# Kernel tuning notes

Hardware: AMD Instinct MI355X
Metric: run time of the kernel (lower is better)

Reference implementation:

```python
import jax, jax.numpy as jnp
import numpy as np
from jax import lax

B, T, N, D = 8, 64, 197, 768
HID = 4
K_FRAME, K_TOKEN = 8, 49
LAMBDA_COV, LAMBDA_SCORE = 1.0, 0.5
LN_EPS = 1e-5


def setup_inputs() -> dict:
    key = jax.random.key(0)
    k = jax.random.split(key, 5)
    x = jax.random.normal(k[0], (B, T, N, D), jnp.float32)
    mask = jax.random.uniform(k[1], (B, T, N), jnp.float32)
    ln_gamma = jnp.ones((D,), jnp.float32)
    ln_beta = jnp.zeros((D,), jnp.float32)
    W1 = jax.random.normal(k[2], (D, HID * D), jnp.float32) * 0.02
    b1 = jnp.zeros((HID * D,), jnp.float32)
    W2 = jax.random.normal(k[3], (HID * D, 1), jnp.float32) * 0.02
    b2 = jnp.zeros((1,), jnp.float32)
    return {"x": x, "mask": mask, "ln_gamma": ln_gamma, "ln_beta": ln_beta,
            "W1": W1, "b1": b1, "W2": W2, "b2": b2}


def _facility_location(frame_repr, score, valid, k):
    # cosine similarity between frames (F.normalize eps = 1e-12)
    fn = frame_repr / jnp.clip(jnp.linalg.norm(frame_repr, axis=-1, keepdims=True), 1e-12)
    sim = jnp.einsum('bid,bjd->bij', fn, fn)  # [B,T,T]
    Bb, Tt = score.shape

    def step(carry, _):
        best_cover, chosen = carry  # [B,T], [B,T] bool
        # coverage gain per candidate j: sum_i max(best[i], sim[i,j]) - best[i]
        cov_gain = jnp.maximum(best_cover[:, :, None], sim).sum(1) - best_cover.sum(1, keepdims=True)
        total = LAMBDA_COV * cov_gain + LAMBDA_SCORE * score
        total = jnp.where(valid & (~chosen), total, -jnp.inf)
        j = jnp.argmax(total, axis=1)  # [B]
        sim_j = jnp.take_along_axis(sim, j[:, None, None], axis=2)[..., 0]  # [B,T]
        best_cover = jnp.maximum(best_cover, sim_j)
        chosen = chosen.at[jnp.arange(Bb), j].set(True)
        return (best_cover, chosen), j

    init = (jnp.zeros((Bb, Tt), frame_repr.dtype), jnp.zeros((Bb, Tt), bool))
    (_, chosen), js = lax.scan(step, init, None, length=k)
    return js.T, chosen.astype(frame_repr.dtype)  # frame_idx [B,k], frame_mask [B,T]


def _kcenter(X, valid, k):
    # X [N,D], valid [N] bool; greedy k-center (farthest point sampling)
    d0 = jnp.where(valid, (X * X).sum(-1), -jnp.inf)
    first = jnp.argmax(d0)

    def dist_to(i):
        diff = X - X[i]
        return jnp.sqrt((diff * diff).sum(-1))

    min_dist = jnp.where(valid, dist_to(first), -1.0)

    def step(md, _):
        cand = jnp.argmax(md)
        md = jnp.where(valid, jnp.minimum(md, dist_to(cand)), -1.0)
        return md, cand

    _, rest = lax.scan(step, min_dist, None, length=k - 1)
    return jnp.concatenate([first[None], rest])


def _forward(x, mask, ln_gamma, ln_beta, W1, b1, W2, b2):
    # masked mean frame representation (use_cls=False path)
    denom = jnp.clip(mask.sum(2), 1e-6)                      # [B,T]
    frame_repr = (x * mask[..., None]).sum(2) / denom[..., None]  # [B,T,D]
    valid_frame = denom > 0

    # score head: LayerNorm -> Linear -> GELU(exact) -> Linear
    mu = frame_repr.mean(-1, keepdims=True)
    var = ((frame_repr - mu) ** 2).mean(-1, keepdims=True)
    h = (frame_repr - mu) / jnp.sqrt(var + LN_EPS) * ln_gamma + ln_beta
    h = jax.nn.gelu(h @ W1 + b1, approximate=False)
    score = (h @ W2 + b2)[..., 0]                            # [B,T]

    # selection is index-valued: no gradient flows through it (as in torch)
    frame_idx, frame_mask = _facility_location(
        lax.stop_gradient(frame_repr), lax.stop_gradient(score), valid_frame, K_FRAME)

    Xf = jnp.take_along_axis(x, frame_idx[:, :, None, None], axis=1)   # [B,K,N,D]
    mf = jnp.take_along_axis(mask, frame_idx[:, :, None], axis=1) > 0.5  # [B,K,N]

    token_idx = jax.vmap(jax.vmap(lambda Xs, vs: _kcenter(Xs, vs, K_TOKEN)))(
        lax.stop_gradient(Xf), mf)                           # [B,K,Kt]

    b_ar = jnp.arange(x.shape[0])
    token_mask = jnp.zeros(mask.shape, x.dtype).at[
        b_ar[:, None, None], frame_idx[:, :, None], token_idx].set(1.0)

    z = jnp.take_along_axis(Xf, token_idx[..., None], axis=2)  # [B,K,Kt,D]
    return z, frame_idx, token_idx, frame_mask, token_mask


def reference(x, mask, ln_gamma, ln_beta, W1, b1, W2, b2):
    return _forward(x, mask, ln_gamma, ln_beta, W1, b1, W2, b2)
```

## Files before the change

kernel.cpp:

```cpp
#include <hip/hip_runtime.h>
#include <math.h>

#define B_ 8
#define T_ 64
#define N_ 197
#define D_ 768
#define HIDD_ 3072
#define KF_ 8
#define KT_ 49
#define GSTRIDE 200

#define Z_SZ    (B_*KF_*KT_*D_)
#define FI_OFF  (Z_SZ)
#define TI_OFF  (FI_OFF + B_*KF_)
#define FM_OFF  (TI_OFF + B_*KF_*KT_)
#define TM_OFF  (FM_OFF + B_*T_)
#define TM_SZ   (B_*T_*N_)

#define WS_SCOREP  0
#define WS_FN64    98304
#define WS_H32     (WS_FN64 + 3145728)
#define WS_VALID   (WS_H32 + 1572864)
#define WS_FIDX    (WS_VALID + 2048)
#define WS_SIM     (WS_FIDX + 256)
#define WS_G       (WS_SIM + 262144)

__global__ __launch_bounds__(256) void kA(const float* __restrict__ x,
                                          const float* __restrict__ mask,
                                          const float* __restrict__ gamma,
                                          const float* __restrict__ beta,
                                          double* __restrict__ fn64,
                                          float* __restrict__ h32,
                                          int* __restrict__ validw) {
  const int row = blockIdx.x;
  const int tid = threadIdx.x;
  __shared__ float  ms[N_];
  __shared__ double red[256];
  __shared__ double sh_denom, sh_mu, sh_sd, sh_nrm;
  const float* xr = x + (size_t)row * (N_ * D_);

  if (tid < N_) ms[tid] = mask[(size_t)row * N_ + tid];
  __syncthreads();

  red[tid] = (tid < N_) ? (double)ms[tid] : 0.0;
  __syncthreads();
  for (int s = 128; s > 0; s >>= 1) { if (tid < s) red[tid] += red[tid + s]; __syncthreads(); }
  if (tid == 0) { double d = red[0]; sh_denom = (d > 1e-6) ? d : 1e-6; }
  __syncthreads();
  const double dn = sh_denom;

  double a0 = 0.0, a1 = 0.0, a2 = 0.0, a3 = 0.0;
  if (tid < 192) {
    const float* px = xr + tid * 4;
#pragma unroll 4
    for (int n = 0; n < N_; n++) {
      const double mv = (double)ms[n];
      const float4 v = *(const float4*)(px + (size_t)n * D_);
      a0 += (double)v.x * mv;
      a1 += (double)v.y * mv;
      a2 += (double)v.z * mv;
      a3 += (double)v.w * mv;
    }
  }
  const double f0 = a0 / dn, f1 = a1 / dn, f2 = a2 / dn, f3 = a3 / dn;

  red[tid] = (tid < 192) ? (f0 + f1 + f2 + f3) : 0.0; __syncthreads();
  for (int s = 128; s > 0; s >>= 1) { if (tid < s) red[tid] += red[tid + s]; __syncthreads(); }
  if (tid == 0) sh_mu = red[0] / (double)D_;
  __syncthreads();
  const double mu = sh_mu;

  red[tid] = (tid < 192) ? (f0 * f0 + f1 * f1 + f2 * f2 + f3 * f3) : 0.0; __syncthreads();
  for (int s = 128; s > 0; s >>= 1) { if (tid < s) red[tid] += red[tid + s]; __syncthreads(); }
  if (tid == 0) { double nr = sqrt(red[0]); sh_nrm = (nr > 1e-12) ? nr : 1e-12; }
  __syncthreads();

  red[tid] = (tid < 192) ? ((f0 - mu) * (f0 - mu) + (f1 - mu) * (f1 - mu) +
                            (f2 - mu) * (f2 - mu) + (f3 - mu) * (f3 - mu)) : 0.0;
  __syncthreads();
  for (int s = 128; s > 0; s >>= 1) { if (tid < s) red[tid] += red[tid + s]; __syncthreads(); }
  if (tid == 0) sh_sd = sqrt(red[0] / (double)D_ + 1e-5);
  __syncthreads();
  const double sd = sh_sd, nrm = sh_nrm;

  if (tid < 192) {
    const size_t base = (size_t)row * D_;
    const float4 g  = ((const float4*)gamma)[tid];
    const float4 be = ((const float4*)beta)[tid];
    float4 hv;
    hv.x = (float)((f0 - mu) / sd * (double)g.x + (double)be.x);
    hv.y = (float)((f1 - mu) / sd * (double)g.y + (double)be.y);
    hv.z = (float)((f2 - mu) / sd * (double)g.z + (double)be.z);
    hv.w = (float)((f3 - mu) / sd * (double)g.w + (double)be.w);
    *(float4*)(h32 + base + tid * 4) = hv;
    double2* fp = (double2*)(fn64 + base + tid * 4);
    fp[0] = make_double2(f0 / nrm, f1 / nrm);
    fp[1] = make_double2(f2 / nrm, f3 / nrm);
  }
  if (tid == 0) validw[row] = 1;
}

__global__ __launch_bounds__(256) void kSB(const double* __restrict__ fn64,
                                           double* __restrict__ simG,
                                           const float* __restrict__ h32,
                                           const float* __restrict__ W1,
                                           const float* __restrict__ b1,
                                           const float* __restrict__ W2,
                                           double* __restrict__ scorep) {
  __shared__ char smem[42496] __attribute__((aligned(16)));
  const int tid = threadIdx.x;

  if (blockIdx.x < 32) {
    const int b    = blockIdx.x >> 2;
    const int tile = blockIdx.x & 3;
    const int ty = tid >> 4;
    const int tx = tid & 15;
    double* As = (double*)smem;
    double* Bs = (double*)(smem + 8704);
    double acc[4] = {0.0, 0.0, 0.0, 0.0};

    for (int kc = 0; kc < 12; kc++) {
#pragma unroll
      for (int it = 0; it < 4; it++) {
        const int idx = (it << 8) + tid;
        const int row = idx >> 6, kk = idx & 63;
        As[kk * 17 + row] = fn64[((size_t)(b * T_ + tile * 16 + row)) * D_ + kc * 64 + kk];
      }
#pragma unroll
      for (int it = 0; it < 16; it++) {
        const int idx = (it << 8) + tid;
        const int row = idx >> 6, kk = idx & 63;
        Bs[kk * 66 + row] = fn64[((size_t)(b * T_ + row)) * D_ + kc * 64 + kk];
      }
      __syncthreads();
#pragma unroll 8
      for (int kk = 0; kk < 64; kk++) {
        const double a = As[kk * 17 + ty];
        const double* bp = Bs + kk * 66 + tx * 4;
        acc[0] += a * bp[0];
        acc[1] += a * bp[1];
        acc[2] += a * bp[2];
        acc[3] += a * bp[3];
      }
      __syncthreads();
    }
    double* o = simG + ((size_t)b * 64 + tile * 16 + ty) * 64 + tx * 4;
    o[0] = acc[0]; o[1] = acc[1]; o[2] = acc[2]; o[3] = acc[3];
  } else {
    const int bid2 = blockIdx.x - 32;
    const int nb = bid2 % 24;
    const int n0 = nb * 128;
    const int m0 = (bid2 / 24) * 32;
    const int tx = tid & 31;
    const int ty = tid >> 5;
    float* As = (float*)smem;
    float* Bs = (float*)(smem + 9216);
    float acc[4][4];
#pragma unroll
    for (int r = 0; r < 4; r++)
#pragma unroll
      for (int c = 0; c < 4; c++) acc[r][c] = 0.0f;

    for (int kc = 0; kc < 12; kc++) {
      const int k0 = kc * 64;
#pragma unroll
      for (int it = 0; it < 8; it++) {
        int idx = tid + (it << 8);
        int k = idx & 63, m = idx >> 6;
        As[k * 36 + m] = h32[(size_t)(m0 + m) * D_ + k0 + k];
      }
#pragma unroll
      for (int it = 0; it < 8; it++) {
        int idx = tid + (it << 8);
        int k = idx >> 5, n4 = idx & 31;
        const float4 v = *(const float4*)(W1 + (size_t)(k0 + k) * HIDD_ + n0 + (n4 << 2));
        *(float4*)(Bs + k * 128 + (n4 << 2)) = v;
      }
      __syncthreads();
#pragma unroll 16
      for (int kk = 0; kk < 64; kk++) {
        float4 av = *(const float4*)(As + kk * 36 + ty * 4);
        float4 bv = *(const float4*)(Bs + kk * 128 + tx * 4);
        const float a[4] = {av.x, av.y, av.z, av.w};
        const float bb[4] = {bv.x, bv.y, bv.z, bv.w};
#pragma unroll
        for (int r = 0; r < 4; r++)
#pragma unroll
          for (int c = 0; c < 4; c++) acc[r][c] += a[r] * bb[c];
      }
      __syncthreads();
    }

    double part[4] = {0.0, 0.0, 0.0, 0.0};
#pragma unroll
    for (int r = 0; r < 4; r++) {
#pragma unroll
      for (int c = 0; c < 4; c++) {
        const int gn = n0 + tx * 4 + c;
        const double v = (double)(acc[r][c] + b1[gn]);
        const double g = 0.5 * v * (1.0 + erf(v * 0.7071067811865475244));
        part[r] += g * (double)W2[gn];
      }
    }
#pragma unroll
    for (int r = 0; r < 4; r++) {
      double s = part[r];
#pragma unroll
      for (int off = 16; off > 0; off >>= 1) s += __shfl_down(s, off, 32);
      if (tx == 0) scorep[(size_t)(m0 + ty * 4 + r) * 24 + nb] = s;
    }
  }
}

__global__ __launch_bounds__(256) void kD(const double* __restrict__ simG,
                                          const double* __restrict__ scorep,
                                          const float* __restrict__ b2,
                                          int* __restrict__ fidxw,
                                          float* __restrict__ out_fidx,
                                          float* __restrict__ out_fmask) {
  const int b = blockIdx.x;
  const int tid = threadIdx.x;
  __shared__ double sim[64 * 64];

  const double2* sp = (const double2*)(simG + (size_t)b * 4096);
#pragma unroll
  for (int it = 0; it < 8; it++) {
    const int idx = (it << 8) + tid;
    ((double2*)sim)[idx] = sp[idx];
  }
  __syncthreads();

  if (tid < 64) {
    double s = 0.0;
    const double* pp = scorep + (size_t)(b * T_ + tid) * 24;
    for (int q = 0; q < 24; q++) s += pp[q];
    const double half_score = 0.5 * (s + (double)b2[0]);

    double bc_r = 0.0;
    int chosen_r = 0;

    for (int step = 0; step < KF_; step++) {
      double gsum = 0.0;
      for (int ii = 0; ii < 64; ii++) {
        const double bcv = __shfl(bc_r, ii, 64);
        gsum += fmax(bcv, sim[ii * 64 + tid]);
      }
      double tot = gsum + half_score;
      if (chosen_r) tot = -INFINITY;

      double bv = tot; int bi = tid;
#pragma unroll
      for (int off = 1; off < 64; off <<= 1) {
        const double ov = __shfl_xor(bv, off, 64);
        const int    oi = __shfl_xor(bi, off, 64);
        if (ov > bv || (ov == bv && oi < bi)) { bv = ov; bi = oi; }
      }
      bc_r = fmax(bc_r, sim[bi * 64 + tid]);
      if (tid == bi) chosen_r = 1;
      if (tid == 0) {
        fidxw[b * KF_ + step] = bi;
        out_fidx[b * KF_ + step] = (float)bi;
      }
    }
    out_fmask[b * T_ + tid] = chosen_r ? 1.0f : 0.0f;
  }
}

__global__ __launch_bounds__(256) void kG(const float* __restrict__ x,
                                          const int* __restrict__ fidxw,
                                          double* __restrict__ G) {
  static const int TIa[10] = {0,0,0,0,1,1,1,2,2,3};
  static const int TJa[10] = {0,1,2,3,1,2,3,2,3,3};
  const int bid  = blockIdx.x;
  const int xcd  = bid & 7;
  const int slot = bid >> 3;
  const int p    = xcd + 8 * (slot / 10);
  const int t    = slot % 10;
  const int ti = TIa[t], tj = TJa[t];
  const int b  = p >> 3;
  const int fi = fidxw[p];
  const float* X = x + ((size_t)(b * T_ + fi)) * (N_ * D_);
  double* Gp = G + (size_t)p * (GSTRIDE * GSTRIDE);

  __shared__ double As[32 * 70];
  __shared__ double Bs[32 * 70];
  const int tid = threadIdx.x;
  const int tx = tid & 15;
  const int ty = tid >> 4;
  const bool diag = (ti == tj);
  const double* Bsel = diag ? As : Bs;
  double acc[4][4];
#pragma unroll
  for (int r = 0; r < 4; r++)
#pragma unroll
    for (int c = 0; c < 4; c++) acc[r][c] = 0.0;

  for (int kc = 0; kc < 24; kc++) {
#pragma unroll
    for (int it = 0; it < 2; it++) {
      const int idx = (it << 8) + tid;
      const int row = idx >> 3;
      const int kg  = idx & 7;
      const int gra = ti * 64 + row;
      const int ra = (gra < N_) ? gra : (N_ - 1);
      const float4 va = *(const float4*)(X + (size_t)ra * D_ + kc * 32 + kg * 4);
      As[(kg * 4 + 0) * 70 + row] = (double)va.x;
      As[(kg * 4 + 1) * 70 + row] = (double)va.y;
      As[(kg * 4 + 2) * 70 + row] = (double)va.z;
      As[(kg * 4 + 3) * 70 + row] = (double)va.w;
      if (!diag) {
        const int grb = tj * 64 + row;
        const int rb = (grb < N_) ? grb : (N_ - 1);
        const float4 vb = *(const float4*)(X + (size_t)rb * D_ + kc * 32 + kg * 4);
        Bs[(kg * 4 + 0) * 70 + row] = (double)vb.x;
        Bs[(kg * 4 + 1) * 70 + row] = (double)vb.y;
        Bs[(kg * 4 + 2) * 70 + row] = (double)vb.z;
        Bs[(kg * 4 + 3) * 70 + row] = (double)vb.w;
      }
    }
    __syncthreads();
#pragma unroll 8
    for (int kk = 0; kk < 32; kk++) {
      const double* ap = As + kk * 70 + ty * 4;
      const double a0 = ap[0], a1 = ap[1], a2 = ap[2], a3 = ap[3];
      const double* bp = Bsel + kk * 70 + tx;
      const double b0 = bp[0], b1 = bp[16], b2 = bp[32], b3 = bp[48];
      acc[0][0] += a0 * b0; acc[0][1] += a0 * b1; acc[0][2] += a0 * b2; acc[0][3] += a0 * b3;
      acc[1][0] += a1 * b0; acc[1][1] += a1 * b1; acc[1][2] += a1 * b2; acc[1][3] += a1 * b3;
      acc[2][0] += a2 * b0; acc[2][1] += a2 * b1; acc[2][2] += a2 * b2; acc[2][3] += a2 * b3;
      acc[3][0] += a3 * b0; acc[3][1] += a3 * b1; acc[3][2] += a3 * b2; acc[3][3] += a3 * b3;
    }
    __syncthreads();
  }

#pragma unroll
  for (int r = 0; r < 4; r++) {
    const int gi = ti * 64 + ty * 4 + r;
#pragma unroll
    for (int c = 0; c < 4; c++) {
      const int gj = tj * 64 + c * 16 + tx;
      if (gi < N_ && gj < N_) {
        Gp[(size_t)gi * GSTRIDE + gj] = acc[r][c];
        if (!diag) Gp[(size_t)gj * GSTRIDE + gi] = acc[r][c];
      }
    }
  }
}

__global__ __launch_bounds__(256) void kE2(const double* __restrict__ G,
                                           const float* __restrict__ mask,
                                           const int* __restrict__ fidxw,
                                           const float* __restrict__ x,
                                           float* __restrict__ out) {
  const int p = blockIdx.x;
  const int b = p >> 3;
  const int fi = fidxw[p];
  const double* Gp = G + (size_t)p * (GSTRIDE * GSTRIDE);
  const float* mrow = mask + (size_t)(b * T_ + fi) * N_;
  const float* X = x + ((size_t)(b * T_ + fi)) * (N_ * D_);
  const int tid = threadIdx.x;

  __shared__ int toksS[KT_];

  if (tid < 64) {
    const int l = tid;
    double gd[4]; int vld[4]; double md[4];
#pragma unroll
    for (int q = 0; q < 4; q++) {
      const int pt = l + 64 * q;
      const bool live = pt < N_;
      gd[q] = live ? Gp[(size_t)pt * GSTRIDE + pt] : 0.0;
      vld[q] = (live && (mrow[live ? pt : 0] > 0.5f)) ? 1 : 0;
      md[q] = -INFINITY;
    }

    double bv = vld[0] ? gd[0] : -INFINITY;
    int bi = l;
#pragma unroll
    for (int q = 1; q < 4; q++) {
      const double v = vld[q] ? gd[q] : -INFINITY;
      if (v > bv) { bv = v; bi = l + 64 * q; }
    }
#pragma unroll
    for (int off = 1; off < 64; off <<= 1) {
      const double ov = __shfl_xor(bv, off, 64);
      const int    oi = __shfl_xor(bi, off, 64);
      if (ov > bv || (ov == bv && oi < bi)) { bv = ov; bi = oi; }
    }
    int cand = bi;
    if (l == 0) toksS[0] = cand;

    for (int k = 1; k < KT_; k++) {
      const size_t rowbase = (size_t)cand * GSTRIDE;
      const double g0 = Gp[rowbase + l];
      const double g1 = Gp[rowbase + l + 64];
      const double g2 = Gp[rowbase + l + 128];
      const int cq = cand >> 6, cl = cand & 63;
      const double gsel = (cq == 0) ? gd[0] : (cq == 1) ? gd[1]
                        : (cq == 2) ? gd[2] : gd[3];
      const double gdc = __shfl(gsel, cl, 64);
      const double d0 = sqrt(fmax(gd[0] + gdc - 2.0 * g0, 0.0));
      const double d1 = sqrt(fmax(gd[1] + gdc - 2.0 * g1, 0.0));
      const double d2 = sqrt(fmax(gd[2] + gdc - 2.0 * g2, 0.0));
      md[0] = vld[0] ? ((k == 1) ? d0 : fmin(md[0], d0)) : -1.0;
      md[1] = vld[1] ? ((k == 1) ? d1 : fmin(md[1], d1)) : -1.0;
      md[2] = vld[2] ? ((k == 1) ? d2 : fmin(md[2], d2)) : -1.0;
      if (l + 192 < N_) {
        const double g3 = Gp[rowbase + l + 192];
        const double d3 = sqrt(fmax(gd[3] + gdc - 2.0 * g3, 0.0));
        md[3] = vld[3] ? ((k == 1) ? d3 : fmin(md[3], d3)) : -1.0;
      }

      bv = md[0]; bi = l;
      if (md[1] > bv) { bv = md[1]; bi = l + 64; }
      if (md[2] > bv) { bv = md[2]; bi = l + 128; }
      if (md[3] > bv) { bv = md[3]; bi = l + 192; }
#pragma unroll
      for (int off = 1; off < 64; off <<= 1) {
        const double ov = __shfl_xor(bv, off, 64);
        const int    oi = __shfl_xor(bi, off, 64);
        if (ov > bv || (ov == bv && oi < bi)) { bv = ov; bi = oi; }
      }
      cand = bi;
      if (l == 0) toksS[k] = cand;
    }
  }
  __syncthreads();

  if (tid < KT_) {
    const int tok = toksS[tid];
    out[TI_OFF + p * KT_ + tid] = (float)tok;
    out[TM_OFF + (size_t)(b * T_ + fi) * N_ + tok] = 1.0f;
  }
  if (tid < 192) {
    for (int r = 0; r < KT_; r++) {
      const float4 v = *(const float4*)(X + (size_t)toksS[r] * D_ + tid * 4);
      *(float4*)(out + ((size_t)(p * KT_ + r)) * D_ + tid * 4) = v;
    }
  }
}

extern "C" void kernel_launch(void* const* d_in, const int* in_sizes, int n_in,
                              void* d_out, int out_size, void* d_ws, size_t ws_size,
                              hipStream_t stream) {
  (void)in_sizes; (void)n_in; (void)ws_size; (void)out_size;
  const float* x     = (const float*)d_in[0];
  const float* mask  = (const float*)d_in[1];
  const float* gamma = (const float*)d_in[2];
  const float* beta  = (const float*)d_in[3];
  const float* W1    = (const float*)d_in[4];
  const float* b1    = (const float*)d_in[5];
  const float* W2    = (const float*)d_in[6];
  const float* b2    = (const float*)d_in[7];
  float* out = (float*)d_out;
  char* ws = (char*)d_ws;

  double* scorep = (double*)(ws + WS_SCOREP);
  double* fn64   = (double*)(ws + WS_FN64);
  float*  h32    = (float*)(ws + WS_H32);
  int*    validw = (int*)(ws + WS_VALID);
  int*    fidxw  = (int*)(ws + WS_FIDX);
  double* simG   = (double*)(ws + WS_SIM);
  double* G      = (double*)(ws + WS_G);

  hipMemsetAsync(out + TM_OFF, 0, (size_t)TM_SZ * sizeof(float), stream);

  kA<<<B_ * T_, 256, 0, stream>>>(x, mask, gamma, beta, fn64, h32, validw);
  kSB<<<32 + (HIDD_ / 128) * ((B_ * T_) / 32), 256, 0, stream>>>(
      fn64, simG, h32, W1, b1, W2, scorep);
  kD<<<B_, 256, 0, stream>>>(simG, scorep, b2, fidxw, out + FI_OFF, out + FM_OFF);
  kG<<<B_ * KF_ * 10, 256, 0, stream>>>(x, fidxw, G);
  kE2<<<B_ * KF_, 256, 0, stream>>>(G, mask, fidxw, x, out);
}
```

Baseline: 758.1 us.

## Use FP64 MFMA for token Gram tiles and use all threads in frame pooling

```diff
diff --git a/kernel.cpp b/kernel.cpp
--- a/kernel.cpp
+++ b/kernel.cpp
@@ -9,6 +9,8 @@
 #define KF_ 8
 #define KT_ 49
 #define GSTRIDE 200
+
+typedef double dbl4 __attribute__((ext_vector_type(4)));
 
 #define Z_SZ    (B_*KF_*KT_*D_)
 #define FI_OFF  (Z_SZ)
@@ -49,53 +51,48 @@
   __syncthreads();
   const double dn = sh_denom;
 
-  double a0 = 0.0, a1 = 0.0, a2 = 0.0, a3 = 0.0;
-  if (tid < 192) {
-    const float* px = xr + tid * 4;
+  double a0 = 0.0, a1 = 0.0, a2 = 0.0;
+  {
+    const float* px = xr + tid * 3;
 #pragma unroll 4
     for (int n = 0; n < N_; n++) {
       const double mv = (double)ms[n];
-      const float4 v = *(const float4*)(px + (size_t)n * D_);
-      a0 += (double)v.x * mv;
-      a1 += (double)v.y * mv;
-      a2 += (double)v.z * mv;
-      a3 += (double)v.w * mv;
-    }
-  }
-  const double f0 = a0 / dn, f1 = a1 / dn, f2 = a2 / dn, f3 = a3 / dn;
-
-  red[tid] = (tid < 192) ? (f0 + f1 + f2 + f3) : 0.0; __syncthreads();
+      const float* q = px + (size_t)n * D_;
+      a0 += (double)q[0] * mv;
+      a1 += (double)q[1] * mv;
+      a2 += (double)q[2] * mv;
+    }
+  }
+  const double f0 = a0 / dn, f1 = a1 / dn, f2 = a2 / dn;
+
+  red[tid] = f0 + f1 + f2; __syncthreads();
   for (int s = 128; s > 0; s >>= 1) { if (tid < s) red[tid] += red[tid + s]; __syncthreads(); }
   if (tid == 0) sh_mu = red[0] / (double)D_;
   __syncthreads();
   const double mu = sh_mu;
 
-  red[tid] = (tid < 192) ? (f0 * f0 + f1 * f1 + f2 * f2 + f3 * f3) : 0.0; __syncthreads();
+  red[tid] = f0 * f0 + f1 * f1 + f2 * f2; __syncthreads();
   for (int s = 128; s > 0; s >>= 1) { if (tid < s) red[tid] += red[tid + s]; __syncthreads(); }
   if (tid == 0) { double nr = sqrt(red[0]); sh_nrm = (nr > 1e-12) ? nr : 1e-12; }
   __syncthreads();
 
-  red[tid] = (tid < 192) ? ((f0 - mu) * (f0 - mu) + (f1 - mu) * (f1 - mu) +
-                            (f2 - mu) * (f2 - mu) + (f3 - mu) * (f3 - mu)) : 0.0;
+  red[tid] = (f0 - mu) * (f0 - mu) + (f1 - mu) * (f1 - mu) + (f2 - mu) * (f2 - mu);
   __syncthreads();
   for (int s = 128; s > 0; s >>= 1) { if (tid < s) red[tid] += red[tid + s]; __syncthreads(); }
   if (tid == 0) sh_sd = sqrt(red[0] / (double)D_ + 1e-5);
   __syncthreads();
   const double sd = sh_sd, nrm = sh_nrm;
 
-  if (tid < 192) {
-    const size_t base = (size_t)row * D_;
-    const float4 g  = ((const float4*)gamma)[tid];
-    const float4 be = ((const float4*)beta)[tid];
-    float4 hv;
-    hv.x = (float)((f0 - mu) / sd * (double)g.x + (double)be.x);
-    hv.y = (float)((f1 - mu) / sd * (double)g.y + (double)be.y);
-    hv.z = (float)((f2 - mu) / sd * (double)g.z + (double)be.z);
-    hv.w = (float)((f3 - mu) / sd * (double)g.w + (double)be.w);
-    *(float4*)(h32 + base + tid * 4) = hv;
-    double2* fp = (double2*)(fn64 + base + tid * 4);
-    fp[0] = make_double2(f0 / nrm, f1 / nrm);
-    fp[1] = make_double2(f2 / nrm, f3 / nrm);
+  {
+    const size_t base = (size_t)row * D_ + tid * 3;
+    const float g0 = gamma[tid * 3 + 0], g1 = gamma[tid * 3 + 1], g2 = gamma[tid * 3 + 2];
+    const float e0 = beta[tid * 3 + 0],  e1 = beta[tid * 3 + 1],  e2 = beta[tid * 3 + 2];
+    h32[base + 0] = (float)((f0 - mu) / sd * (double)g0 + (double)e0);
+    h32[base + 1] = (float)((f1 - mu) / sd * (double)g1 + (double)e1);
+    h32[base + 2] = (float)((f2 - mu) / sd * (double)g2 + (double)e2);
+    fn64[base + 0] = f0 / nrm;
+    fn64[base + 1] = f1 / nrm;
+    fn64[base + 2] = f2 / nrm;
   }
   if (tid == 0) validw[row] = 1;
 }
@@ -282,18 +279,32 @@
   const float* X = x + ((size_t)(b * T_ + fi)) * (N_ * D_);
   double* Gp = G + (size_t)p * (GSTRIDE * GSTRIDE);
 
-  __shared__ double As[32 * 70];
-  __shared__ double Bs[32 * 70];
-  const int tid = threadIdx.x;
-  const int tx = tid & 15;
-  const int ty = tid >> 4;
+  __shared__ float As[64 * 36];
+  __shared__ float Bs[64 * 36];
+  const int tid  = threadIdx.x;
+  const int w    = tid >> 6;
+  const int lane = tid & 63;
+  const int lr   = lane & 15;
+  const int lk   = lane >> 4;
   const bool diag = (ti == tj);
-  const double* Bsel = diag ? As : Bs;
-  double acc[4][4];
-#pragma unroll
-  for (int r = 0; r < 4; r++)
-#pragma unroll
-    for (int c = 0; c < 4; c++) acc[r][c] = 0.0;
+  const float* Bsel = diag ? As : Bs;
+
+  dbl4 pz = {0.0, 0.0, 0.0, 0.0};
+  const dbl4 p1 = __builtin_amdgcn_mfma_f64_16x16x4f64((double)lr, 1.0, pz, 0, 0, 0);
+  const dbl4 p2 = __builtin_amdgcn_mfma_f64_16x16x4f64(1.0, (double)lr, pz, 0, 0, 0);
+  int iofs[4], jofs[4];
+#pragma unroll
+  for (int e = 0; e < 4; e++) {
+    iofs[e] = (int)(p1[e] * 0.25 + 0.5);
+    jofs[e] = (int)(p2[e] * 0.25 + 0.5);
+  }
+
+  dbl4 acc0 = {0.0, 0.0, 0.0, 0.0};
+  dbl4 acc1 = {0.0, 0.0, 0.0, 0.0};
+  dbl4 acc2 = {0.0, 0.0, 0.0, 0.0};
+  dbl4 acc3 = {0.0, 0.0, 0.0, 0.0};
+
+  const int arow = w * 16 + lr;
 
   for (int kc = 0; kc < 24; kc++) {
 #pragma unroll
@@ -302,46 +313,43 @@
       const int row = idx >> 3;
       const int kg  = idx & 7;
       const int gra = ti * 64 + row;
-      const int ra = (gra < N_) ? gra : (N_ - 1);
+      const int ra  = (gra < N_) ? gra : (N_ - 1);
       const float4 va = *(const float4*)(X + (size_t)ra * D_ + kc * 32 + kg * 4);
-      As[(kg * 4 + 0) * 70 + row] = (double)va.x;
-      As[(kg * 4 + 1) * 70 + row] = (double)va.y;
-      As[(kg * 4 + 2) * 70 + row] = (double)va.z;
-      As[(kg * 4 + 3) * 70 + row] = (double)va.w;
+      *(float4*)(As + row * 36 + kg * 4) = va;
       if (!diag) {
         const int grb = tj * 64 + row;
-        const int rb = (grb < N_) ? grb : (N_ - 1);
+        const int rb  = (grb < N_) ? grb : (N_ - 1);
         const float4 vb = *(const float4*)(X + (size_t)rb * D_ + kc * 32 + kg * 4);
-        Bs[(kg * 4 + 0) * 70 + row] = (double)vb.x;
-        Bs[(kg * 4 + 1) * 70 + row] = (double)vb.y;
-        Bs[(kg * 4 + 2) * 70 + row] = (double)vb.z;
-        Bs[(kg * 4 + 3) * 70 + row] = (double)vb.w;
+        *(float4*)(Bs + row * 36 + kg * 4) = vb;
       }
     }
     __syncthreads();
-#pragma unroll 8
-    for (int kk = 0; kk < 32; kk++) {
-      const double* ap = As + kk * 70 + ty * 4;
-      const double a0 = ap[0], a1 = ap[1], a2 = ap[2], a3 = ap[3];
-      const double* bp = Bsel + kk * 70 + tx;
-      const double b0 = bp[0], b1 = bp[16], b2 = bp[32], b3 = bp[48];
-      acc[0][0] += a0 * b0; acc[0][1] += a0 * b1; acc[0][2] += a0 * b2; acc[0][3] += a0 * b3;
-      acc[1][0] += a1 * b0; acc[1][1] += a1 * b1; acc[1][2] += a1 * b2; acc[1][3] += a1 * b3;
-      acc[2][0] += a2 * b0; acc[2][1] += a2 * b1; acc[2][2] += a2 * b2; acc[2][3] += a2 * b3;
-      acc[3][0] += a3 * b0; acc[3][1] += a3 * b1; acc[3][2] += a3 * b2; acc[3][3] += a3 * b3;
+#pragma unroll
+    for (int k4 = 0; k4 < 8; k4++) {
+      const int kbase = k4 * 4 + lk;
+      const double av  = (double)As[arow * 36 + kbase];
+      const double bv0 = (double)Bsel[(lr     ) * 36 + kbase];
+      const double bv1 = (double)Bsel[(16 + lr) * 36 + kbase];
+      const double bv2 = (double)Bsel[(32 + lr) * 36 + kbase];
+      const double bv3 = (double)Bsel[(48 + lr) * 36 + kbase];
+      acc0 = __builtin_amdgcn_mfma_f64_16x16x4f64(av, bv0, acc0, 0, 0, 0);
+      acc1 = __builtin_amdgcn_mfma_f64_16x16x4f64(av, bv1, acc1, 0, 0, 0);
+      acc2 = __builtin_amdgcn_mfma_f64_16x16x4f64(av, bv2, acc2, 0, 0, 0);
+      acc3 = __builtin_amdgcn_mfma_f64_16x16x4f64(av, bv3, acc3, 0, 0, 0);
     }
     __syncthreads();
   }
 
 #pragma unroll
-  for (int r = 0; r < 4; r++) {
-    const int gi = ti * 64 + ty * 4 + r;
-#pragma unroll
-    for (int c = 0; c < 4; c++) {
-      const int gj = tj * 64 + c * 16 + tx;
+  for (int ct = 0; ct < 4; ct++) {
+    const dbl4 a = (ct == 0) ? acc0 : (ct == 1) ? acc1 : (ct == 2) ? acc2 : acc3;
+#pragma unroll
+    for (int e = 0; e < 4; e++) {
+      const int gi = ti * 64 + w * 16 + iofs[e];
+      const int gj = tj * 64 + ct * 16 + jofs[e];
       if (gi < N_ && gj < N_) {
-        Gp[(size_t)gi * GSTRIDE + gj] = acc[r][c];
-        if (!diag) Gp[(size_t)gj * GSTRIDE + gi] = acc[r][c];
+        Gp[(size_t)gi * GSTRIDE + gj] = a[e];
+        if (!diag) Gp[(size_t)gj * GSTRIDE + gi] = a[e];
       }
     }
   }
```

Measured after the change: 706.5 us. 1.07x faster.
